# Performance work log

Hardware: AMD Instinct MI355X
Metric: run time of the kernel (lower is better)

The kernel has to match this reference:

```python
import jax, jax.numpy as jnp
import numpy as np

B, N, DEG = 32, 1024, 8
E = B * N * DEG
NT = B * N
F_IN, HID, EDIM, NR, HD = 64, 128, 16, 16, 4
NEG = 0.2  # leaky_relu negative slope (alpha)
K1 = int(np.ceil(0.8 * N))    # 820 kept nodes per graph after pool1
K2 = int(np.ceil(0.8 * K1))   # 656 kept nodes per graph after pool2


def setup_inputs() -> dict:
    key = jax.random.key(0)
    ks = jax.random.split(key, 20)
    nrm = lambda i, shp, s=0.05: jax.random.normal(ks[i], shp, jnp.float32) * s
    x = jax.random.normal(ks[0], (NT, F_IN), jnp.float32)
    off = (jnp.arange(B) * N)[:, None]
    src = (jax.random.randint(ks[1], (B, N * DEG), 0, N) + off).reshape(-1)
    dst = (jax.random.randint(ks[2], (B, N * DEG), 0, N) + off).reshape(-1)
    edge_index = jnp.stack([src, dst]).astype(jnp.int32)
    edge_attr = jax.random.normal(ks[3], (E, EDIM), jnp.float32)
    action = jax.random.normal(ks[4], (B, NR), jnp.float32)
    return dict(
        x=x, edge_attr=edge_attr, action=action,
        W1l=nrm(5, (F_IN, HD * HID)), b1l=jnp.zeros(HD * HID),
        W1r=nrm(6, (F_IN, HD * HID)), b1r=jnp.zeros(HD * HID),
        W1e=nrm(7, (EDIM, HD * HID)), att1=nrm(8, (HD, HID)), bias1=jnp.zeros(HID),
        W2l=nrm(9, (HID, HD * HID)), b2l=jnp.zeros(HD * HID),
        W2r=nrm(10, (HID, HD * HID)), b2r=jnp.zeros(HD * HID),
        W2e=nrm(11, (EDIM, HD * HID)), att2=nrm(12, (HD, HID)), bias2=jnp.zeros(HID),
        p1=nrm(13, (HID,), 0.1), p2=nrm(14, (HID,), 0.1),
        Wf1=nrm(15, (2 * HID + NR, HID)), bf1=jnp.zeros(HID),
        Wf2=nrm(16, (HID, HID)), bf2=jnp.zeros(HID),
        Wf3=nrm(17, (HID, 1), 0.003), bf3=jnp.zeros(1),
        edge_index=edge_index,
    )


def _gatv2(x, edge_index, edge_attr, edge_mask, Wl, bl, Wr, br, We, att, bias):
    # PyG GATv2Conv, concat=False (mean over heads), eval mode (no dropout).
    src, dst = edge_index[0], edge_index[1]
    n = x.shape[0]
    xl = (x @ Wl + bl).reshape(n, HD, HID)   # source transform (x_j)
    xr = (x @ Wr + br).reshape(n, HD, HID)   # target transform (x_i)
    ef = (edge_attr @ We).reshape(-1, HD, HID)
    m = jax.nn.leaky_relu(xl[src] + xr[dst] + ef, NEG)          # [E,H,C]
    logits = jnp.where(edge_mask[:, None], (m * att).sum(-1), -1e9)  # [E,H]
    mx = jax.ops.segment_max(logits, dst, num_segments=n)
    a = jnp.exp(logits - mx[dst])
    den = jax.ops.segment_sum(a, dst, num_segments=n)
    alpha = (a / (den[dst] + 1e-16)) * edge_mask[:, None]       # softmax per dst, masked edges zeroed
    out = jax.ops.segment_sum(xl[src] * alpha[..., None], dst, num_segments=n)
    return out.mean(axis=1) + bias


def _topk(x, node_mask, p, k):
    # PyG TopKPooling: score = x@p/||p||, gate = tanh(score), keep top-k per graph.
    score = (x @ p) / (jnp.linalg.norm(p) + 1e-16)
    gate = jnp.tanh(score)
    s = jnp.where(node_mask, score, -jnp.inf).reshape(B, N)
    idx = jax.lax.top_k(s, k)[1]                                # [B,k]
    keep = jnp.zeros((B, N), bool).at[jnp.arange(B)[:, None], idx].set(True).reshape(-1)
    return x * gate[:, None], keep


def reference(x, edge_attr, action, W1l, b1l, W1r, b1r, W1e, att1, bias1,
              W2l, b2l, W2r, b2r, W2e, att2, bias2, p1, p2,
              Wf1, bf1, Wf2, bf2, Wf3, bf3, edge_index):
    src, dst = edge_index[0], edge_index[1]
    em0 = jnp.ones((E,), bool)
    h = jax.nn.relu(_gatv2(x, edge_index, edge_attr, em0,
                           W1l, b1l, W1r, b1r, W1e, att1, bias1))
    h, keep1 = _topk(h, jnp.ones((NT,), bool), p1, K1)
    em1 = keep1[src] & keep1[dst]
    h = jax.nn.relu(_gatv2(h, edge_index, edge_attr, em1,
                           W2l, b2l, W2r, b2r, W2e, att2, bias2))
    h, keep2 = _topk(h, keep1, p2, K2)
    hb = h.reshape(B, N, HID)
    mb = keep2.reshape(B, N)[..., None]
    gmx = jnp.where(mb, hb, -jnp.inf).max(axis=1)               # global max pool over kept nodes
    gav = (hb * mb).sum(axis=1) / K2                            # global mean pool (K2 kept per graph)
    z = jnp.concatenate([gmx, gav, action], axis=1)             # [B, 2*HID+NR]
    z = jax.nn.relu(z @ Wf1 + bf1)
    z = jax.nn.relu(z @ Wf2 + bf2)
    return z @ Wf3 + bf3
```

## Files before the change

kernel.cpp:

```cpp
#include <hip/hip_runtime.h>
#include <math.h>

#define NTN 32768
#define NBG 32
#define NN  1024
#define EE  262144
#define FIN 64
#define HIDC 128
#define HD  4
#define HC  512
#define EDIM 16
#define NR  16
#define KP1 820
#define KP2 656
#define NEGS 0.2f

template<int K>
__global__ __launch_bounds__(256) void gemm_node(const float* __restrict__ A,
                                                 const float* __restrict__ W,
                                                 const float* __restrict__ b,
                                                 const float* __restrict__ gs,
                                                 float* __restrict__ C) {
    __shared__ float a_s[K][16];
    __shared__ float g_s[16];
    int t = threadIdx.x;
    int row0 = blockIdx.x * 16;
    if (t < 16) g_s[t] = gs ? tanhf(gs[row0 + t]) : 1.0f;
    __syncthreads();
    for (int i = t; i < 16 * K; i += 256) {
        int r = i / K, k = i % K;
        a_s[k][r] = A[(size_t)(row0 + r) * K + k] * g_s[r];
    }
    __syncthreads();
    int c0 = t, c1 = t + 256;
    float acc0[16], acc1[16];
    float bb0 = b[c0], bb1 = b[c1];
    #pragma unroll
    for (int r = 0; r < 16; r++) { acc0[r] = bb0; acc1[r] = bb1; }
    for (int k = 0; k < K; k++) {
        float w0 = W[(size_t)k * HC + c0], w1 = W[(size_t)k * HC + c1];
        const float4* ap = (const float4*)&a_s[k][0];
        float4 A0 = ap[0], A1 = ap[1], A2 = ap[2], A3 = ap[3];
        float av[16] = {A0.x, A0.y, A0.z, A0.w, A1.x, A1.y, A1.z, A1.w,
                        A2.x, A2.y, A2.z, A2.w, A3.x, A3.y, A3.z, A3.w};
        #pragma unroll
        for (int r = 0; r < 16; r++) { acc0[r] += av[r] * w0; acc1[r] += av[r] * w1; }
    }
    for (int r = 0; r < 16; r++) {
        C[(size_t)(row0 + r) * HC + c0] = acc0[r];
        C[(size_t)(row0 + r) * HC + c1] = acc1[r];
    }
}

__global__ void edge_hist(const int* __restrict__ dst, const int* __restrict__ src,
                          const int* __restrict__ keep, int* __restrict__ deg) {
    int e = blockIdx.x * 256 + threadIdx.x;
    if (e < EE) {
        if (keep && (!keep[src[e]] || !keep[dst[e]])) return;
        atomicAdd(&deg[dst[e]], 1);
    }
}

__global__ __launch_bounds__(1024) void scan_deg(const int* __restrict__ deg,
                                                 int* __restrict__ off, int* __restrict__ cur) {
    __shared__ int s[1024];
    int t = threadIdx.x;
    int base = t * 32;
    int local[32];
    int sum = 0;
    #pragma unroll
    for (int i = 0; i < 32; i++) { local[i] = deg[base + i]; sum += local[i]; }
    s[t] = sum;
    for (int o = 1; o < 1024; o <<= 1) {
        __syncthreads();
        int v = (t >= o) ? s[t - o] : 0;
        __syncthreads();
        s[t] += v;
    }
    __syncthreads();
    int run = s[t] - sum;
    #pragma unroll
    for (int i = 0; i < 32; i++) { off[base + i] = run; cur[base + i] = run; run += local[i]; }
    if (t == 1023) off[NTN] = s[1023];
}

__global__ void edge_scatter(const int* __restrict__ dst, const int* __restrict__ src,
                             const int* __restrict__ keep, int* __restrict__ cur,
                             int* __restrict__ ebuf, int* __restrict__ esrc) {
    int e = blockIdx.x * 256 + threadIdx.x;
    if (e < EE) {
        if (keep && (!keep[src[e]] || !keep[dst[e]])) return;
        int p = atomicAdd(&cur[dst[e]], 1);
        ebuf[p] = e;
        esrc[p] = src[e];
    }
}

__global__ __launch_bounds__(256) void gat_dst(
        const float* __restrict__ xl, const float* __restrict__ xr,
        const float* __restrict__ ea, const float* __restrict__ We,
        const float* __restrict__ att, const float* __restrict__ bias,
        const int* __restrict__ ebuf, const int* __restrict__ esrc,
        const int* __restrict__ off,
        float* __restrict__ out) {
    int d = blockIdx.x;
    int t = threadIdx.x;
    int w = t >> 6, lane = t & 63;
    int c = w * HIDC + lane * 2;
    float we0[EDIM], we1[EDIM];
    #pragma unroll
    for (int k = 0; k < EDIM; k++) {
        we0[k] = We[(size_t)k * HC + c];
        we1[k] = We[(size_t)k * HC + c + 1];
    }
    float at0 = att[c], at1 = att[c + 1];
    float2 xrv = *(const float2*)&xr[(size_t)d * HC + c];
    int e0 = off[d], e1 = off[d + 1];
    float m = -3e38f, den = 0.f, acc0 = 0.f, acc1 = 0.f;
    for (int ei = e0; ei < e1; ei++) {
        int e = ebuf[ei];
        int s = esrc[ei];
        const float4* eap = (const float4*)(ea + (size_t)e * EDIM);
        float4 E0 = eap[0], E1 = eap[1], E2 = eap[2], E3 = eap[3];
        float2 xlv = *(const float2*)&xl[(size_t)s * HC + c];
        float ev[16] = {E0.x, E0.y, E0.z, E0.w, E1.x, E1.y, E1.z, E1.w,
                        E2.x, E2.y, E2.z, E2.w, E3.x, E3.y, E3.z, E3.w};
        float ef0 = 0.f, ef1 = 0.f;
        #pragma unroll
        for (int k = 0; k < EDIM; k++) { ef0 += ev[k] * we0[k]; ef1 += ev[k] * we1[k]; }
        float v0 = xlv.x + xrv.x + ef0; v0 = v0 > 0.f ? v0 : NEGS * v0;
        float v1 = xlv.y + xrv.y + ef1; v1 = v1 > 0.f ? v1 : NEGS * v1;
        float p = v0 * at0 + v1 * at1;
        #pragma unroll
        for (int sft = 32; sft; sft >>= 1) p += __shfl_xor(p, sft, 64);
        if (p > m) {
            float sc = __expf(m - p);
            den = den * sc + 1.f;
            acc0 = acc0 * sc + xlv.x;
            acc1 = acc1 * sc + xlv.y;
            m = p;
        } else {
            float wt = __expf(p - m);
            den += wt;
            acc0 += wt * xlv.x;
            acc1 += wt * xlv.y;
        }
    }
    __shared__ float red[HC];
    float inv = 1.f / (den + 1e-16f);
    red[c] = acc0 * inv;
    red[c + 1] = acc1 * inv;
    __syncthreads();
    if (t < HIDC) {
        float v = (red[t] + red[t + 128] + red[t + 256] + red[t + 384]) * 0.25f + bias[t];
        out[(size_t)d * HIDC + t] = fmaxf(v, 0.f);
    }
}

__global__ __launch_bounds__(256) void score_nodes(const float* __restrict__ h,
                                                   const float* __restrict__ p,
                                                   float* __restrict__ score) {
    __shared__ float pS[HIDC];
    __shared__ float invn;
    int t = threadIdx.x;
    if (t < HIDC) pS[t] = p[t];
    __syncthreads();
    if (t == 0) {
        float s = 0.f;
        for (int i = 0; i < HIDC; i++) s += pS[i] * pS[i];
        invn = 1.f / (sqrtf(s) + 1e-16f);
    }
    __syncthreads();
    int w = t >> 6, lane = t & 63;
    float p0 = pS[lane * 2], p1 = pS[lane * 2 + 1];
    float iv = invn;
    for (int j = 0; j < 8; j++) {
        int n = blockIdx.x * 32 + w * 8 + j;
        float2 hv = *(const float2*)&h[(size_t)n * HIDC + lane * 2];
        float v = hv.x * p0 + hv.y * p1;
        #pragma unroll
        for (int sft = 32; sft; sft >>= 1) v += __shfl_xor(v, sft, 64);
        if (lane == 0) score[n] = v * iv;
    }
}

__global__ __launch_bounds__(512) void topk_sel(const float* __restrict__ score,
                                                const int* __restrict__ mask, int k,
                                                int* __restrict__ keep) {
    __shared__ float v[NN];
    __shared__ short id[NN];
    int g = blockIdx.x, t = threadIdx.x;
    for (int i = t; i < NN; i += 512) {
        int n = g * NN + i;
        bool mk = mask ? (mask[n] != 0) : true;
        v[i] = mk ? score[n] : -INFINITY;
        id[i] = (short)i;
    }
    __syncthreads();
    for (int kk = 2; kk <= NN; kk <<= 1) {
        for (int j = kk >> 1; j > 0; j >>= 1) {
            #pragma unroll 2
            for (int i = t; i < NN; i += 512) {
                int ixj = i ^ j;
                if (ixj > i) {
                    bool up = ((i & kk) == 0);
                    float a = v[i], b2 = v[ixj];
                    short ia = id[i], ib = id[ixj];
                    bool aFirst = (a > b2) || (a == b2 && ia < ib);
                    if (up ? !aFirst : aFirst) { v[i] = b2; v[ixj] = a; id[i] = ib; id[ixj] = ia; }
                }
            }
            __syncthreads();
        }
    }
    for (int i = t; i < NN; i += 512) keep[g * NN + id[i]] = (i < k) ? 1 : 0;
}

__global__ __launch_bounds__(512) void gpool(const float* __restrict__ h,
                                             const int* __restrict__ keep,
                                             const float* __restrict__ score,
                                             const float* __restrict__ action,
                                             float* __restrict__ z) {
    int g = blockIdx.x, t = threadIdx.x;
    int c = t & 127, ch = t >> 7;
    __shared__ float gt_s[NN];
    __shared__ char kp_s[NN];
    __shared__ float smx[4][HIDC], ssm[4][HIDC];
    for (int i = t; i < NN; i += 512) {
        int n = g * NN + i;
        int kk = keep[n];
        kp_s[i] = (char)kk;
        gt_s[i] = kk ? tanhf(score[n]) : 0.f;
    }
    __syncthreads();
    float mx = -INFINITY, sm = 0.f;
    for (int n = ch * 256; n < ch * 256 + 256; n++) {
        if (kp_s[n]) {
            float v = h[(size_t)(g * NN + n) * HIDC + c] * gt_s[n];
            mx = fmaxf(mx, v);
            sm += v;
        }
    }
    smx[ch][c] = mx; ssm[ch][c] = sm;
    __syncthreads();
    if (t < HIDC) {
        mx = fmaxf(fmaxf(smx[0][t], smx[1][t]), fmaxf(smx[2][t], smx[3][t]));
        sm = ssm[0][t] + ssm[1][t] + ssm[2][t] + ssm[3][t];
        z[g * 272 + t] = mx;
        z[g * 272 + 128 + t] = sm / (float)KP2;
        if (t < NR) z[g * 272 + 256 + t] = action[g * NR + t];
    }
}

__global__ __launch_bounds__(128) void mlp(const float* __restrict__ z,
                                           const float* __restrict__ Wf1, const float* __restrict__ bf1,
                                           const float* __restrict__ Wf2, const float* __restrict__ bf2,
                                           const float* __restrict__ Wf3, const float* __restrict__ bf3,
                                           float* __restrict__ out) {
    int g = blockIdx.x, t = threadIdx.x;
    __shared__ float zs[272], z1[HIDC], z2[HIDC], r[HIDC];
    for (int i = t; i < 272; i += 128) zs[i] = z[g * 272 + i];
    __syncthreads();
    float a = bf1[t];
    for (int k = 0; k < 272; k++) a += zs[k] * Wf1[(size_t)k * HIDC + t];
    z1[t] = fmaxf(a, 0.f);
    __syncthreads();
    a = bf2[t];
    for (int k = 0; k < HIDC; k++) a += z1[k] * Wf2[(size_t)k * HIDC + t];
    z2[t] = fmaxf(a, 0.f);
    __syncthreads();
    r[t] = z2[t] * Wf3[t];
    __syncthreads();
    for (int s = 64; s; s >>= 1) { if (t < s) r[t] += r[t + s]; __syncthreads(); }
    if (t == 0) out[g] = r[0] + bf3[0];
}

extern "C" void kernel_launch(void* const* d_in, const int* in_sizes, int n_in,
                              void* d_out, int out_size, void* d_ws, size_t ws_size,
                              hipStream_t stream) {
    const float* x    = (const float*)d_in[0];
    const float* ea   = (const float*)d_in[1];
    const float* act  = (const float*)d_in[2];
    const float* W1l  = (const float*)d_in[3];
    const float* b1l  = (const float*)d_in[4];
    const float* W1r  = (const float*)d_in[5];
    const float* b1r  = (const float*)d_in[6];
    const float* W1e  = (const float*)d_in[7];
    const float* att1 = (const float*)d_in[8];
    const float* bias1= (const float*)d_in[9];
    const float* W2l  = (const float*)d_in[10];
    const float* b2l  = (const float*)d_in[11];
    const float* W2r  = (const float*)d_in[12];
    const float* b2r  = (const float*)d_in[13];
    const float* W2e  = (const float*)d_in[14];
    const float* att2 = (const float*)d_in[15];
    const float* bias2= (const float*)d_in[16];
    const float* p1   = (const float*)d_in[17];
    const float* p2   = (const float*)d_in[18];
    const float* Wf1  = (const float*)d_in[19];
    const float* bf1  = (const float*)d_in[20];
    const float* Wf2  = (const float*)d_in[21];
    const float* bf2  = (const float*)d_in[22];
    const float* Wf3  = (const float*)d_in[23];
    const float* bf3  = (const float*)d_in[24];
    const int*   eix  = (const int*)d_in[25];
    const int* srcA = eix;
    const int* dstA = eix + EE;

    float* ws    = (float*)d_ws;
    float* xl    = ws;
    float* xr    = xl + (size_t)NTN * HC;
    float* h     = xr + (size_t)NTN * HC;
    float* score1= h + (size_t)NTN * HIDC;
    float* score2= score1 + NTN;
    float* zbuf  = score2 + NTN;
    int* keep1 = (int*)(zbuf + NBG * 272);
    int* keep2 = keep1 + NTN;
    int* deg   = keep2 + NTN;
    int* off   = deg + NTN;
    int* cur   = off + NTN + 1;
    int* ebuf  = cur + NTN;
    int* esrc  = ebuf + EE;
    int* deg2  = esrc + EE;
    int* off2  = deg2 + NTN;
    int* cur2  = off2 + NTN + 1;
    int* ebuf2 = cur2 + NTN;
    int* esrc2 = ebuf2 + EE;

    hipMemsetAsync(deg, 0, NTN * sizeof(int), stream);
    edge_hist<<<EE / 256, 256, 0, stream>>>(dstA, srcA, nullptr, deg);
    scan_deg<<<1, 1024, 0, stream>>>(deg, off, cur);
    edge_scatter<<<EE / 256, 256, 0, stream>>>(dstA, srcA, nullptr, cur, ebuf, esrc);

    gemm_node<FIN><<<NTN / 16, 256, 0, stream>>>(x, W1l, b1l, nullptr, xl);
    gemm_node<FIN><<<NTN / 16, 256, 0, stream>>>(x, W1r, b1r, nullptr, xr);
    gat_dst<<<NTN, 256, 0, stream>>>(xl, xr, ea, W1e, att1, bias1, ebuf, esrc, off, h);

    score_nodes<<<NTN / 32, 256, 0, stream>>>(h, p1, score1);
    topk_sel<<<NBG, 512, 0, stream>>>(score1, nullptr, KP1, keep1);

    hipMemsetAsync(deg2, 0, NTN * sizeof(int), stream);
    edge_hist<<<EE / 256, 256, 0, stream>>>(dstA, srcA, keep1, deg2);
    scan_deg<<<1, 1024, 0, stream>>>(deg2, off2, cur2);
    edge_scatter<<<EE / 256, 256, 0, stream>>>(dstA, srcA, keep1, cur2, ebuf2, esrc2);

    gemm_node<HIDC><<<NTN / 16, 256, 0, stream>>>(h, W2l, b2l, score1, xl);
    gemm_node<HIDC><<<NTN / 16, 256, 0, stream>>>(h, W2r, b2r, score1, xr);
    gat_dst<<<NTN, 256, 0, stream>>>(xl, xr, ea, W2e, att2, bias2, ebuf2, esrc2, off2, h);

    score_nodes<<<NTN / 32, 256, 0, stream>>>(h, p2, score2);
    topk_sel<<<NBG, 512, 0, stream>>>(score2, keep1, KP2, keep2);

    gpool<<<NBG, 512, 0, stream>>>(h, keep2, score2, act, zbuf);
    mlp<<<NBG, 128, 0, stream>>>(zbuf, Wf1, bf1, Wf2, bf2, Wf3, bf3, (float*)d_out);
}
```

Measured before the change: 640.2 us.

## Fuse left/right GEMMs, pre-permute edge attrs, fuse scoring into GAT kernel

After: 833.1 us. 1.3x slower.

```diff
diff --git a/kernel.cpp b/kernel.cpp
--- a/kernel.cpp
+++ b/kernel.cpp
@@ -14,13 +14,18 @@
 #define KP1 820
 #define KP2 656
 #define NEGS 0.2f
+#define NPB 8
+#define CHUNK 64
 
 template<int K>
-__global__ __launch_bounds__(256) void gemm_node(const float* __restrict__ A,
-                                                 const float* __restrict__ W,
-                                                 const float* __restrict__ b,
-                                                 const float* __restrict__ gs,
-                                                 float* __restrict__ C) {
+__global__ __launch_bounds__(256) void gemm_node2(const float* __restrict__ A,
+                                                  const float* __restrict__ Wl,
+                                                  const float* __restrict__ bl,
+                                                  const float* __restrict__ Wr,
+                                                  const float* __restrict__ br,
+                                                  const float* __restrict__ gs,
+                                                  float* __restrict__ Cl,
+                                                  float* __restrict__ Cr) {
     __shared__ float a_s[K][16];
     __shared__ float g_s[16];
     int t = threadIdx.x;
@@ -33,22 +38,28 @@
     }
     __syncthreads();
     int c0 = t, c1 = t + 256;
-    float acc0[16], acc1[16];
-    float bb0 = b[c0], bb1 = b[c1];
+    float accl0[16], accl1[16], accr0[16], accr1[16];
+    float bl0 = bl[c0], bl1 = bl[c1], br0 = br[c0], br1 = br[c1];
     #pragma unroll
-    for (int r = 0; r < 16; r++) { acc0[r] = bb0; acc1[r] = bb1; }
+    for (int r = 0; r < 16; r++) { accl0[r] = bl0; accl1[r] = bl1; accr0[r] = br0; accr1[r] = br1; }
     for (int k = 0; k < K; k++) {
-        float w0 = W[(size_t)k * HC + c0], w1 = W[(size_t)k * HC + c1];
+        float wl0 = Wl[(size_t)k * HC + c0], wl1 = Wl[(size_t)k * HC + c1];
+        float wr0 = Wr[(size_t)k * HC + c0], wr1 = Wr[(size_t)k * HC + c1];
         const float4* ap = (const float4*)&a_s[k][0];
         float4 A0 = ap[0], A1 = ap[1], A2 = ap[2], A3 = ap[3];
         float av[16] = {A0.x, A0.y, A0.z, A0.w, A1.x, A1.y, A1.z, A1.w,
                         A2.x, A2.y, A2.z, A2.w, A3.x, A3.y, A3.z, A3.w};
         #pragma unroll
-        for (int r = 0; r < 16; r++) { acc0[r] += av[r] * w0; acc1[r] += av[r] * w1; }
+        for (int r = 0; r < 16; r++) {
+            accl0[r] += av[r] * wl0; accl1[r] += av[r] * wl1;
+            accr0[r] += av[r] * wr0; accr1[r] += av[r] * wr1;
+        }
     }
     for (int r = 0; r < 16; r++) {
-        C[(size_t)(row0 + r) * HC + c0] = acc0[r];
-        C[(size_t)(row0 + r) * HC + c1] = acc1[r];
+        Cl[(size_t)(row0 + r) * HC + c0] = accl0[r];
+        Cl[(size_t)(row0 + r) * HC + c1] = accl1[r];
+        Cr[(size_t)(row0 + r) * HC + c0] = accr0[r];
+        Cr[(size_t)(row0 + r) * HC + c1] = accr1[r];
     }
 }
 
@@ -85,28 +96,36 @@
 }
 
 __global__ void edge_scatter(const int* __restrict__ dst, const int* __restrict__ src,
-                             const int* __restrict__ keep, int* __restrict__ cur,
-                             int* __restrict__ ebuf, int* __restrict__ esrc) {
+                             const int* __restrict__ keep, const float* __restrict__ ea,
+                             int* __restrict__ cur,
+                             int* __restrict__ esrc, float* __restrict__ eaP) {
     int e = blockIdx.x * 256 + threadIdx.x;
     if (e < EE) {
         if (keep && (!keep[src[e]] || !keep[dst[e]])) return;
         int p = atomicAdd(&cur[dst[e]], 1);
-        ebuf[p] = e;
         esrc[p] = src[e];
+        const float4* s4 = (const float4*)(ea + (size_t)e * EDIM);
+        float4* d4 = (float4*)(eaP + (size_t)p * EDIM);
+        d4[0] = s4[0]; d4[1] = s4[1]; d4[2] = s4[2]; d4[3] = s4[3];
     }
 }
 
 __global__ __launch_bounds__(256) void gat_dst(
         const float* __restrict__ xl, const float* __restrict__ xr,
-        const float* __restrict__ ea, const float* __restrict__ We,
+        const float* __restrict__ eaP, const float* __restrict__ We,
         const float* __restrict__ att, const float* __restrict__ bias,
-        const int* __restrict__ ebuf, const int* __restrict__ esrc,
-        const int* __restrict__ off,
-        float* __restrict__ out) {
-    int d = blockIdx.x;
+        const float* __restrict__ pvec,
+        const int* __restrict__ esrc, const int* __restrict__ off,
+        float* __restrict__ out, float* __restrict__ score) {
     int t = threadIdx.x;
     int w = t >> 6, lane = t & 63;
     int c = w * HIDC + lane * 2;
+    __shared__ float logitS[HD][CHUNK];
+    __shared__ int   srcS[HD][CHUNK];
+    __shared__ float red[2][HC];
+    __shared__ float red2[2][HIDC];
+    __shared__ float biasS[HIDC], pS[HIDC];
+    __shared__ float invn_s;
     float we0[EDIM], we1[EDIM];
     #pragma unroll
     for (int k = 0; k < EDIM; k++) {
@@ -114,73 +133,74 @@
         we1[k] = We[(size_t)k * HC + c + 1];
     }
     float at0 = att[c], at1 = att[c + 1];
-    float2 xrv = *(const float2*)&xr[(size_t)d * HC + c];
-    int e0 = off[d], e1 = off[d + 1];
-    float m = -3e38f, den = 0.f, acc0 = 0.f, acc1 = 0.f;
-    for (int ei = e0; ei < e1; ei++) {
-        int e = ebuf[ei];
-        int s = esrc[ei];
-        const float4* eap = (const float4*)(ea + (size_t)e * EDIM);
-        float4 E0 = eap[0], E1 = eap[1], E2 = eap[2], E3 = eap[3];
-        float2 xlv = *(const float2*)&xl[(size_t)s * HC + c];
-        float ev[16] = {E0.x, E0.y, E0.z, E0.w, E1.x, E1.y, E1.z, E1.w,
-                        E2.x, E2.y, E2.z, E2.w, E3.x, E3.y, E3.z, E3.w};
-        float ef0 = 0.f, ef1 = 0.f;
+    if (t < HIDC) { biasS[t] = bias[t]; pS[t] = pvec[t]; }
+    __syncthreads();
+    if (t < 64) {
+        float s = pS[t] * pS[t] + pS[t + 64] * pS[t + 64];
         #pragma unroll
-        for (int k = 0; k < EDIM; k++) { ef0 += ev[k] * we0[k]; ef1 += ev[k] * we1[k]; }
-        float v0 = xlv.x + xrv.x + ef0; v0 = v0 > 0.f ? v0 : NEGS * v0;
-        float v1 = xlv.y + xrv.y + ef1; v1 = v1 > 0.f ? v1 : NEGS * v1;
-        float p = v0 * at0 + v1 * at1;
-        #pragma unroll
-        for (int sft = 32; sft; sft >>= 1) p += __shfl_xor(p, sft, 64);
-        if (p > m) {
-            float sc = __expf(m - p);
-            den = den * sc + 1.f;
-            acc0 = acc0 * sc + xlv.x;
-            acc1 = acc1 * sc + xlv.y;
-            m = p;
-        } else {
-            float wt = __expf(p - m);
-            den += wt;
-            acc0 += wt * xlv.x;
-            acc1 += wt * xlv.y;
-        }
-    }
-    __shared__ float red[HC];
-    float inv = 1.f / (den + 1e-16f);
-    red[c] = acc0 * inv;
-    red[c + 1] = acc1 * inv;
-    __syncthreads();
-    if (t < HIDC) {
-        float v = (red[t] + red[t + 128] + red[t + 256] + red[t + 384]) * 0.25f + bias[t];
-        out[(size_t)d * HIDC + t] = fmaxf(v, 0.f);
-    }
-}
-
-__global__ __launch_bounds__(256) void score_nodes(const float* __restrict__ h,
-                                                   const float* __restrict__ p,
-                                                   float* __restrict__ score) {
-    __shared__ float pS[HIDC];
-    __shared__ float invn;
-    int t = threadIdx.x;
-    if (t < HIDC) pS[t] = p[t];
-    __syncthreads();
-    if (t == 0) {
-        float s = 0.f;
-        for (int i = 0; i < HIDC; i++) s += pS[i] * pS[i];
-        invn = 1.f / (sqrtf(s) + 1e-16f);
-    }
-    __syncthreads();
-    int w = t >> 6, lane = t & 63;
-    float p0 = pS[lane * 2], p1 = pS[lane * 2 + 1];
-    float iv = invn;
-    for (int j = 0; j < 8; j++) {
-        int n = blockIdx.x * 32 + w * 8 + j;
-        float2 hv = *(const float2*)&h[(size_t)n * HIDC + lane * 2];
-        float v = hv.x * p0 + hv.y * p1;
-        #pragma unroll
-        for (int sft = 32; sft; sft >>= 1) v += __shfl_xor(v, sft, 64);
-        if (lane == 0) score[n] = v * iv;
+        for (int sft = 32; sft; sft >>= 1) s += __shfl_xor(s, sft, 64);
+        if (t == 0) invn_s = 1.f / (sqrtf(s) + 1e-16f);
+    }
+    __syncthreads();
+    float invn = invn_s;
+
+    for (int n = 0; n < NPB; n++) {
+        int d = blockIdx.x * NPB + n;
+        float2 xrv = *(const float2*)&xr[((unsigned)d << 9) + c];
+        int e0 = off[d], e1 = off[d + 1];
+        float m = -3e38f, den = 0.f, acc0 = 0.f, acc1 = 0.f;
+        for (int cb = e0; cb < e1; cb += CHUNK) {
+            int ce = cb + CHUNK < e1 ? cb + CHUNK : e1;
+            float mx = -3e38f;
+            for (int ei = cb; ei < ce; ei++) {
+                const float4* eap = (const float4*)(eaP + ((size_t)ei << 4));
+                float4 E0 = eap[0], E1 = eap[1], E2 = eap[2], E3 = eap[3];
+                int s = esrc[ei];
+                float2 xlv = *(const float2*)&xl[((unsigned)s << 9) + c];
+                float ev[16] = {E0.x, E0.y, E0.z, E0.w, E1.x, E1.y, E1.z, E1.w,
+                                E2.x, E2.y, E2.z, E2.w, E3.x, E3.y, E3.z, E3.w};
+                float ef0 = 0.f, ef1 = 0.f;
+                #pragma unroll
+                for (int k = 0; k < EDIM; k++) { ef0 += ev[k] * we0[k]; ef1 += ev[k] * we1[k]; }
+                float v0 = xlv.x + xrv.x + ef0; v0 = v0 > 0.f ? v0 : NEGS * v0;
+                float v1 = xlv.y + xrv.y + ef1; v1 = v1 > 0.f ? v1 : NEGS * v1;
+                float p = v0 * at0 + v1 * at1;
+                #pragma unroll
+                for (int sft = 32; sft; sft >>= 1) p += __shfl_xor(p, sft, 64);
+                if (lane == 0) { logitS[w][ei - cb] = p; srcS[w][ei - cb] = s; }
+                mx = fmaxf(mx, p);
+            }
+            float nm = fmaxf(m, mx);
+            float sc = __expf(m - nm);
+            den *= sc; acc0 *= sc; acc1 *= sc; m = nm;
+            for (int ei = cb; ei < ce; ei++) {
+                float l = logitS[w][ei - cb];
+                int s = srcS[w][ei - cb];
+                float wt = __expf(l - m);
+                float2 xlv = *(const float2*)&xl[((unsigned)s << 9) + c];
+                den += wt;
+                acc0 += wt * xlv.x;
+                acc1 += wt * xlv.y;
+            }
+        }
+        int buf = n & 1;
+        float inv = 1.f / (den + 1e-16f);
+        red[buf][c] = acc0 * inv;
+        red[buf][c + 1] = acc1 * inv;
+        __syncthreads();
+        if (t < HIDC) {
+            float v = (red[buf][t] + red[buf][t + 128] + red[buf][t + 256] + red[buf][t + 384]) * 0.25f + biasS[t];
+            v = fmaxf(v, 0.f);
+            out[((unsigned)d << 7) + t] = v;
+            red2[buf][t] = v * pS[t];
+        }
+        __syncthreads();
+        if (t < 64) {
+            float sv = red2[buf][t] + red2[buf][t + 64];
+            #pragma unroll
+            for (int sft = 32; sft; sft >>= 1) sv += __shfl_xor(sv, sft, 64);
+            if (t == 0) score[d] = sv * invn;
+        }
     }
 }
 
@@ -319,36 +339,32 @@
     int* deg   = keep2 + NTN;
     int* off   = deg + NTN;
     int* cur   = off + NTN + 1;
-    int* ebuf  = cur + NTN;
-    int* esrc  = ebuf + EE;
-    int* deg2  = esrc + EE;
+    int* deg2  = cur + NTN;
     int* off2  = deg2 + NTN;
     int* cur2  = off2 + NTN + 1;
-    int* ebuf2 = cur2 + NTN;
-    int* esrc2 = ebuf2 + EE;
+    int* esrc  = cur2 + NTN;
+    int* esrc2 = esrc + EE;
+    float* eaP  = (float*)(esrc2 + EE);
+    float* eaP2 = eaP + (size_t)EE * EDIM;
 
     hipMemsetAsync(deg, 0, NTN * sizeof(int), stream);
     edge_hist<<<EE / 256, 256, 0, stream>>>(dstA, srcA, nullptr, deg);
     scan_deg<<<1, 1024, 0, stream>>>(deg, off, cur);
-    edge_scatter<<<EE / 256, 256, 0, stream>>>(dstA, srcA, nullptr, cur, ebuf, esrc);
-
-    gemm_node<FIN><<<NTN / 16, 256, 0, stream>>>(x, W1l, b1l, nullptr, xl);
-    gemm_node<FIN><<<NTN / 16, 256, 0, stream>>>(x, W1r, b1r, nullptr, xr);
-    gat_dst<<<NTN, 256, 0, stream>>>(xl, xr, ea, W1e, att1, bias1, ebuf, esrc, off, h);
-
-    score_nodes<<<NTN / 32, 256, 0, stream>>>(h, p1, score1);
+    edge_scatter<<<EE / 256, 256, 0, stream>>>(dstA, srcA, nullptr, ea, cur, esrc, eaP);
+
+    gemm_node2<FIN><<<NTN / 16, 256, 0, stream>>>(x, W1l, b1l, W1r, b1r, nullptr, xl, xr);
+    gat_dst<<<NTN / NPB, 256, 0, stream>>>(xl, xr, eaP, W1e, att1, bias1, p1, esrc, off, h, score1);
+
     topk_sel<<<NBG, 512, 0, stream>>>(score1, nullptr, KP1, keep1);
 
     hipMemsetAsync(deg2, 0, NTN * sizeof(int), stream);
     edge_hist<<<EE / 256, 256, 0, stream>>>(dstA, srcA, keep1, deg2);
     scan_deg<<<1, 1024, 0, stream>>>(deg2, off2, cur2);
-    edge_scatter<<<EE / 256, 256, 0, stream>>>(dstA, srcA, keep1, cur2, ebuf2, esrc2);
-
-    gemm_node<HIDC><<<NTN / 16, 256, 0, stream>>>(h, W2l, b2l, score1, xl);
-    gemm_node<HIDC><<<NTN / 16, 256, 0, stream>>>(h, W2r, b2r, score1, xr);
-    gat_dst<<<NTN, 256, 0, stream>>>(xl, xr, ea, W2e, att2, bias2, ebuf2, esrc2, off2, h);
-
-    score_nodes<<<NTN / 32, 256, 0, stream>>>(h, p2, score2);
+    edge_scatter<<<EE / 256, 256, 0, stream>>>(dstA, srcA, keep1, ea, cur2, esrc2, eaP2);
+
+    gemm_node2<HIDC><<<NTN / 16, 256, 0, stream>>>(h, W2l, b2l, W2r, b2r, score1, xl, xr);
+    gat_dst<<<NTN / NPB, 256, 0, stream>>>(xl, xr, eaP2, W2e, att2, bias2, p2, esrc2, off2, h, score2);
+
     topk_sel<<<NBG, 512, 0, stream>>>(score2, keep1, KP2, keep2);
 
     gpool<<<NBG, 512, 0, stream>>>(h, keep2, score2, act, zbuf);
```
